# Performance work log

Measured on AMD Instinct MI355X. Metric: run time of the kernel, lower is better.

The kernel has to match this reference:

```python
import jax, jax.numpy as jnp
import numpy as np
from math import factorial as fact

H = 32            # hidden channels
NUM_GRAPHS = 128  # number of graphs in the batch (fill_max of `batch`)
SIGMA = 0.1       # gaussian basis width
MUS = jnp.asarray(np.linspace(0.7, 1.7, 10), jnp.float32)
R_CUT = 1.5       # polynomial cutoff radius (p=6)
SL = {0: (0, 1), 1: (1, 4), 2: (4, 9)}  # m-slices per degree in flattened (l,m) layout

# ---- real Clebsch-Gordan coefficients (computed once in numpy) ----

def _cg1(l1, m1, l2, m2, l3, m3):
    if m1 + m2 != m3:
        return 0.0
    pref = ((2 * l3 + 1) * fact(l3 + l1 - l2) * fact(l3 - l1 + l2) * fact(l1 + l2 - l3) / fact(l1 + l2 + l3 + 1)) ** 0.5
    pref *= (fact(l3 + m3) * fact(l3 - m3) * fact(l1 - m1) * fact(l1 + m1) * fact(l2 - m2) * fact(l2 + m2)) ** 0.5
    s = 0.0
    for k in range(0, l1 + l2 - l3 + 1):
        d = [k, l1 + l2 - l3 - k, l1 - m1 - k, l2 + m2 - k, l3 - l2 + m1 + k, l3 - l1 - m2 + k]
        if min(d) < 0:
            continue
        s += (-1.0) ** k / np.prod([float(fact(v)) for v in d])
    return pref * s

def _q(l):  # complex -> real spherical-harmonic basis change
    Q = np.zeros((2 * l + 1, 2 * l + 1), dtype=complex)
    Q[l, l] = 1.0
    for m in range(1, l + 1):
        Q[l + m, l + m] = (-1) ** m / np.sqrt(2)
        Q[l + m, l - m] = 1 / np.sqrt(2)
        Q[l - m, l - m] = 1j / np.sqrt(2)
        Q[l - m, l + m] = -1j * (-1) ** m / np.sqrt(2)
    return Q

def _real_cg(l1, l2, l3):
    Cc = np.zeros((2 * l1 + 1, 2 * l2 + 1, 2 * l3 + 1))
    for m1 in range(-l1, l1 + 1):
        for m2 in range(-l2, l2 + 1):
            m3 = m1 + m2
            if abs(m3) <= l3:
                Cc[m1 + l1, m2 + l2, m3 + l3] = _cg1(l1, m1, l2, m2, l3, m3)
    C = np.einsum('ai,bj,ck,ijk->abc', _q(l1), _q(l2), np.conj(_q(l3)), Cc)
    if np.abs(C.imag).max() > np.abs(C.real).max():
        C = C * (-1j)
    return jnp.asarray(np.real(C), dtype=jnp.float32)

PATHS1 = [(0, 0, 0), (0, 1, 1)]
PATHS2 = [(0, 0, 0), (0, 1, 1), (1, 0, 1), (1, 1, 0), (1, 1, 1), (1, 2, 1)]
PATHS3 = [(0, 0, 0), (1, 1, 0)]
CG = {p: _real_cg(*p) for p in set(PATHS1 + PATHS2 + PATHS3)}

# ---- module math ----

def _ssp(x):  # shifted softplus
    return jax.nn.softplus(x) - jnp.asarray(np.log(2.0), x.dtype)

def _norm_act(h):  # NormAct(ShiftedSoftPlus, L=1): act scalars, gate l=1 vectors by act(norm)/norm
    s = _ssp(h[:, :1, :])
    v = h[:, 1:4, :]
    n = jnp.sqrt(jnp.sum(v * v, axis=1, keepdims=True) + 1e-12)
    return jnp.concatenate([s, v * (_ssp(n) / n)], axis=1)

def _tfn(x, src, dst, edge_sh, w, ew, paths, L_out, channel_wise, N):
    # x: (N, M_in, C_in); per edge: gather x_j, CG tensor product with edge SH,
    # radial weights, cutoff weighting, scatter-sum to destination nodes.
    E = edge_sh.shape[0]
    C_out = w.shape[-1]
    M_out = (L_out + 1) ** 2
    xj = x[src]  # (E, M_in, C_in) edge gather
    msg = jnp.zeros((E, M_out, C_out), x.dtype)
    for p, (l1, l2, l3) in enumerate(paths):
        x1 = xj[:, SL[l1][0]:SL[l1][1], :]          # (E, 2l1+1, C_in)
        y2 = edge_sh[:, SL[l2][0]:SL[l2][1]]        # (E, 2l2+1)
        t = jnp.einsum('abc,eai,eb->eci', CG[(l1, l2, l3)], x1, y2)  # (E, 2l3+1, C_in)
        if channel_wise:
            t = t * w[:, p, None, :]                # (E, P, C) radial weights
        else:
            t = jnp.einsum('eci,eio->eco', t, w[:, p])  # (E, P, C_in, C_out)
        msg = msg.at[:, SL[l3][0]:SL[l3][1], :].add(t * ew[:, None, None])
    return jax.ops.segment_sum(msg, dst, num_segments=N)

def _forward(x, edge_index, edge_sh, edge_len, batch, W1, b1, W2, b2, W3, b3, Wo, bo):
    N = x.shape[0]
    src, dst = edge_index[0], edge_index[1]
    d = edge_len
    emb = jnp.exp(-((d[:, None] - MUS) ** 2) / (2.0 * SIGMA ** 2))  # (E, 10)
    u = d / R_CUT
    ew = jnp.where(u < 1.0, 1.0 - 28.0 * u ** 6 + 48.0 * u ** 7 - 21.0 * u ** 8, 0.0)
    w1 = (emb @ W1 + b1).reshape(-1, 2, 1, H)   # channel_wise=False: (E,P,Cin,Cout)
    w2 = (emb @ W2 + b2).reshape(-1, 6, H)      # channel_wise=True
    w3 = (emb @ W3 + b3).reshape(-1, 2, H)
    h = x[:, None, :]  # (N, 1, 1): L_in=0 scalars
    h = _norm_act(_tfn(h, src, dst, edge_sh, w1, ew, PATHS1, 1, False, N))
    h = _norm_act(_tfn(h, src, dst, edge_sh, w2, ew, PATHS2, 1, True, N))
    h = jax.nn.silu(_tfn(h, src, dst, edge_sh, w3, ew, PATHS3, 0, True, N))
    g = jax.ops.segment_sum(h[:, 0, :], batch, num_segments=NUM_GRAPHS)  # (B, H)
    return jax.nn.softmax(g @ Wo + bo, axis=-1)

def setup_inputs() -> dict:
    N, E = 50000, 800000
    ks = jax.random.split(jax.random.key(0), 16)
    inp = {
        'x': jax.random.normal(ks[0], (N, 1), jnp.float32),
        'edge_index': jax.random.randint(ks[1], (2, E), 0, N),
        'edge_sh': jax.random.normal(ks[2], (E, 9), jnp.float32),
        'edge_len': jax.random.uniform(ks[3], (E,), jnp.float32),
        'batch': jnp.sort(jax.random.randint(ks[4], (N,), 0, NUM_GRAPHS)),
        'W1': jax.random.normal(ks[5], (10, 2 * H), jnp.float32) * 0.1,
        'b1': jnp.zeros((2 * H,), jnp.float32),
        'W2': jax.random.normal(ks[6], (10, 6 * H), jnp.float32) * 0.1,
        'b2': jnp.zeros((6 * H,), jnp.float32),
        'W3': jax.random.normal(ks[7], (10, 2 * H), jnp.float32) * 0.1,
        'b3': jnp.zeros((2 * H,), jnp.float32),
        'Wo': jax.random.normal(ks[8], (H, 8), jnp.float32) * 0.1,
        'bo': jnp.zeros((8,), jnp.float32),
    }
    return inp

def reference(x, edge_sh, edge_len, W1, b1, W2, b2, W3, b3, Wo, bo, edge_index, batch):
    return _forward(x, edge_index, edge_sh, edge_len, batch, W1, b1, W2, b2, W3, b3, Wo, bo)
```

## Files before the change

### kernel.cpp

```cpp
#include <hip/hip_runtime.h>
#include <cmath>
#include <cstring>
#include <complex>

#define HCH 32

struct CGT {
  float c000;
  float c011[9];
  float c101[9];
  float c110[9];
  float c111[27];
  float c121[45];
};

static double factd(int n){ double r=1.0; for(int i=2;i<=n;++i) r*=i; return r; }

static double cg1(int l1,int m1,int l2,int m2,int l3,int m3){
  if(m1+m2!=m3) return 0.0;
  double pref = std::sqrt((2*l3+1)*factd(l3+l1-l2)*factd(l3-l1+l2)*factd(l1+l2-l3)/factd(l1+l2+l3+1));
  pref *= std::sqrt(factd(l3+m3)*factd(l3-m3)*factd(l1-m1)*factd(l1+m1)*factd(l2-m2)*factd(l2+m2));
  double s=0.0;
  for(int k=0;k<=l1+l2-l3;++k){
    int d[6]={k, l1+l2-l3-k, l1-m1-k, l2+m2-k, l3-l2+m1+k, l3-l1-m2+k};
    bool neg=false; for(int i=0;i<6;i++) if(d[i]<0) neg=true;
    if(neg) continue;
    double prod=1.0; for(int i=0;i<6;i++) prod*=factd(d[i]);
    s += ((k&1)? -1.0:1.0)/prod;
  }
  return pref*s;
}

static void qmat(int l, std::complex<double> Q[5][5]){
  for(int i=0;i<5;i++) for(int j=0;j<5;j++) Q[i][j]=0.0;
  Q[l][l]=1.0;
  const double is2 = 1.0/std::sqrt(2.0);
  for(int m=1;m<=l;m++){
    double sgn = (m&1)? -1.0: 1.0;
    Q[l+m][l+m] = sgn*is2;
    Q[l+m][l-m] = is2;
    Q[l-m][l-m] = std::complex<double>(0.0, is2);
    Q[l-m][l+m] = std::complex<double>(0.0, -sgn*is2);
  }
}

static void real_cg(int l1,int l2,int l3, float* out){
  int n1=2*l1+1, n2=2*l2+1, n3=2*l3+1;
  double Cc[5][5][5];
  std::memset(Cc,0,sizeof Cc);
  for(int m1=-l1;m1<=l1;m1++) for(int m2=-l2;m2<=l2;m2++){
    int m3=m1+m2;
    if(m3>=-l3 && m3<=l3) Cc[m1+l1][m2+l2][m3+l3]=cg1(l1,m1,l2,m2,l3,m3);
  }
  std::complex<double> Q1[5][5],Q2[5][5],Q3[5][5];
  qmat(l1,Q1); qmat(l2,Q2); qmat(l3,Q3);
  std::complex<double> C[5][5][5];
  double maxre=0.0, maxim=0.0;
  for(int a=0;a<n1;a++) for(int b=0;b<n2;b++) for(int c=0;c<n3;c++){
    std::complex<double> s=0.0;
    for(int i=0;i<n1;i++) for(int j=0;j<n2;j++) for(int k=0;k<n3;k++){
      double cc=Cc[i][j][k];
      if(cc!=0.0) s += Q1[a][i]*Q2[b][j]*std::conj(Q3[c][k])*cc;
    }
    C[a][b][c]=s;
    maxre=std::max(maxre,std::fabs(s.real()));
    maxim=std::max(maxim,std::fabs(s.imag()));
  }
  bool flip = maxim>maxre;
  for(int a=0;a<n1;a++) for(int b=0;b<n2;b++) for(int c=0;c<n3;c++){
    std::complex<double> v=C[a][b][c];
    if(flip) v *= std::complex<double>(0.0,-1.0);
    out[(a*n2+b)*n3+c]=(float)v.real();
  }
}

static void build_cg(CGT* cg){
  float t000[1];  real_cg(0,0,0,t000); cg->c000=t000[0];
  real_cg(0,1,1,cg->c011);
  real_cg(1,0,1,cg->c101);
  real_cg(1,1,0,cg->c110);
  real_cg(1,1,1,cg->c111);
  real_cg(1,2,1,cg->c121);
}

__device__ __forceinline__ float sspf(float x){
  return fmaxf(x,0.0f) + __logf(1.0f + __expf(-fabsf(x))) - 0.69314718055994530942f;
}

__device__ __forceinline__ float edge_env_inline(float d, float* emb){
#pragma unroll
  for(int k=0;k<10;k++){
    float t = d - (0.7f + (float)k*(1.0f/9.0f));
    emb[k] = __expf(-t*t*50.0f);
  }
  float u = d*(1.0f/1.5f);
  if(u >= 1.0f) return 0.0f;
  float u2=u*u, u3=u2*u, u6=u3*u3, u7=u6*u, u8=u7*u;
  return 1.0f - 28.0f*u6 + 48.0f*u7 - 21.0f*u8;
}

__global__ void deg_kernel(const int* __restrict__ ei, int* __restrict__ deg, int E){
  int e = blockIdx.x*blockDim.x + threadIdx.x;
  if(e >= E) return;
  atomicAdd(&deg[ei[E+e]], 1);
}

__global__ void scanA_kernel(const int* __restrict__ deg, int* __restrict__ rowptr,
                             int* __restrict__ bsum, int N){
  __shared__ int sm[256];
  int t = threadIdx.x, b = blockIdx.x, i = b*256 + t;
  int v = (i < N) ? deg[i] : 0;
  sm[t] = v;
  __syncthreads();
  for(int off=1; off<256; off<<=1){
    int add = (t >= off) ? sm[t-off] : 0;
    __syncthreads();
    sm[t] += add;
    __syncthreads();
  }
  if(i < N) rowptr[i] = sm[t] - v;
  if(t == 255) bsum[b] = sm[255];
}

__global__ void scanB_kernel(int* __restrict__ bsum, int* __restrict__ rowptr, int nb, int N){
  __shared__ int sm[256];
  int t = threadIdx.x;
  int v = (t < nb) ? bsum[t] : 0;
  sm[t] = v;
  __syncthreads();
  for(int off=1; off<256; off<<=1){
    int add = (t >= off) ? sm[t-off] : 0;
    __syncthreads();
    sm[t] += add;
    __syncthreads();
  }
  if(t < nb) bsum[t] = sm[t] - v;
  if(t == 255) rowptr[N] = sm[255];
}

__global__ void scanC_kernel(int* __restrict__ rowptr, const int* __restrict__ bsum, int N){
  int i = blockIdx.x*blockDim.x + threadIdx.x;
  if(i < N) rowptr[i] += bsum[i>>8];
}

__global__ void fill_kernel(const int* __restrict__ ei, const float* __restrict__ elen,
                            const float* __restrict__ sh,
                            const int* __restrict__ rowptr, int* __restrict__ fillc,
                            float* __restrict__ pedge, int E){
  int e = blockIdx.x*blockDim.x + threadIdx.x;
  if(e >= E) return;
  int dst = ei[E+e];
  int p = atomicAdd(&fillc[dst], 1);
  size_t slot = (size_t)rowptr[dst] + p;
  const float* she = sh + (size_t)e*9;
  float4* pd = (float4*)pedge + slot*3;
  pd[0] = make_float4(elen[e], __int_as_float(ei[e]), she[0], she[1]);
  pd[1] = make_float4(she[2], she[3], she[4], she[5]);
  pd[2] = make_float4(she[6], she[7], she[8], 0.f);
}


__global__ __launch_bounds__(256, 4)
void g1_kernel(const float* __restrict__ x,
               const float* __restrict__ pedge,
               const int* __restrict__ rowptr,
               const float* __restrict__ W1, const float* __restrict__ b1,
               float* __restrict__ out, int N, CGT cg){
  int t = blockIdx.x*blockDim.x + threadIdx.x;
  int n = t >> 5, h = t & 31;
  if(n >= N) return;
  int beg = rowptr[n], end = rowptr[n+1];
  float Wr0[10], Wr1[10];
#pragma unroll
  for(int k=0;k<10;k++){ Wr0[k] = W1[k*64 + h]; Wr1[k] = W1[k*64 + HCH + h]; }
  float bb0 = b1[h], bb1 = b1[HCH+h];
  float a0=0.f, a1=0.f, a2=0.f, a3=0.f;
  const float4* pe = (const float4*)pedge;
  for(int i=beg;i<end;i++){
    float4 r0 = pe[(size_t)i*3+0];
    float4 r1 = pe[(size_t)i*3+1];
    float em[10];
    float ew = edge_env_inline(r0.x, em);
    int src = __float_as_int(r0.y);
    float w0 = bb0, w1v = bb1;
#pragma unroll
    for(int k=0;k<10;k++){ w0 += em[k]*Wr0[k]; w1v += em[k]*Wr1[k]; }
    float base = x[src]*ew;
    a0 += cg.c000*base*r0.z*w0;
    float bw = base*w1v;
    a1 += (cg.c011[0]*r0.w + cg.c011[3]*r1.x + cg.c011[6]*r1.y)*bw;
    a2 += (cg.c011[1]*r0.w + cg.c011[4]*r1.x + cg.c011[7]*r1.y)*bw;
    a3 += (cg.c011[2]*r0.w + cg.c011[5]*r1.x + cg.c011[8]*r1.y)*bw;
  }
  float ss = a1*a1 + a2*a2 + a3*a3 + 1e-12f;
  float rn = rsqrtf(ss);
  float sc = sspf(ss*rn)*rn;
  float* p = out + (size_t)n*128;
  p[h]       = sspf(a0);
  p[HCH+h]   = a1*sc;
  p[2*HCH+h] = a2*sc;
  p[3*HCH+h] = a3*sc;
}

__global__ __launch_bounds__(256, 4)
void g2_kernel(const float* __restrict__ hin,
               const float* __restrict__ pedge,
               const int* __restrict__ rowptr,
               const float* __restrict__ W2, const float* __restrict__ b2,
               float* __restrict__ out, int N, CGT cg){
  int t = blockIdx.x*blockDim.x + threadIdx.x;
  int n = t >> 5, h = t & 31;
  if(n >= N) return;
  int beg = rowptr[n], end = rowptr[n+1];
  float Wr[60];
#pragma unroll
  for(int k=0;k<10;k++)
#pragma unroll
    for(int p=0;p<6;p++) Wr[k*6+p] = W2[k*192 + p*HCH + h];
  float bb[6];
#pragma unroll
  for(int p=0;p<6;p++) bb[p] = b2[p*HCH + h];
  float a0=0.f, a1=0.f, a2=0.f, a3=0.f;
  const float4* pe = (const float4*)pedge;
  for(int i=beg;i<end;i++){
    float4 r0 = pe[(size_t)i*3+0];
    float4 r1 = pe[(size_t)i*3+1];
    float4 r2 = pe[(size_t)i*3+2];
    float em[10];
    float ew = edge_env_inline(r0.x, em);
    int src = __float_as_int(r0.y);
    float w_[6];
#pragma unroll
    for(int p=0;p<6;p++) w_[p] = bb[p];
#pragma unroll
    for(int k=0;k<10;k++)
#pragma unroll
      for(int p=0;p<6;p++) w_[p] += em[k]*Wr[k*6+p];
    const float* hn = hin + (size_t)src*128;
    float x0  = hn[h];
    float xv0 = hn[HCH+h], xv1 = hn[2*HCH+h], xv2 = hn[3*HCH+h];
    float s0  = r0.z;
    float sv0 = r0.w, sv1 = r1.x, sv2 = r1.y;
    float s2v[5] = { r1.z, r1.w, r2.x, r2.y, r2.z };

    float m0 = 0.0f, m1 = 0.0f, m2 = 0.0f, m3 = 0.0f;
    m0 += cg.c000 * x0 * s0 * w_[0];
    {
      float xw = x0 * w_[1];
      m1 += (cg.c011[0]*sv0 + cg.c011[3]*sv1 + cg.c011[6]*sv2)*xw;
      m2 += (cg.c011[1]*sv0 + cg.c011[4]*sv1 + cg.c011[7]*sv2)*xw;
      m3 += (cg.c011[2]*sv0 + cg.c011[5]*sv1 + cg.c011[8]*sv2)*xw;
    }
    {
      float sw = s0 * w_[2];
      m1 += (cg.c101[0]*xv0 + cg.c101[3]*xv1 + cg.c101[6]*xv2)*sw;
      m2 += (cg.c101[1]*xv0 + cg.c101[4]*xv1 + cg.c101[7]*xv2)*sw;
      m3 += (cg.c101[2]*xv0 + cg.c101[5]*xv1 + cg.c101[8]*xv2)*sw;
    }
    {
      float tt = cg.c110[0]*xv0*sv0 + cg.c110[1]*xv0*sv1 + cg.c110[2]*xv0*sv2
               + cg.c110[3]*xv1*sv0 + cg.c110[4]*xv1*sv1 + cg.c110[5]*xv1*sv2
               + cg.c110[6]*xv2*sv0 + cg.c110[7]*xv2*sv1 + cg.c110[8]*xv2*sv2;
      m0 += tt * w_[3];
    }
    {
      float xvv[3] = {xv0, xv1, xv2};
      float svv[3] = {sv0, sv1, sv2};
      float t1=0.f, t2=0.f, t3=0.f;
#pragma unroll
      for(int a=0;a<3;a++)
#pragma unroll
        for(int b=0;b<3;b++){
          float xs = xvv[a]*svv[b];
          t1 += cg.c111[(a*3+b)*3+0]*xs;
          t2 += cg.c111[(a*3+b)*3+1]*xs;
          t3 += cg.c111[(a*3+b)*3+2]*xs;
        }
      m1 += t1*w_[4]; m2 += t2*w_[4]; m3 += t3*w_[4];
    }
    {
      float xvv[3] = {xv0, xv1, xv2};
      float t1=0.f, t2=0.f, t3=0.f;
#pragma unroll
      for(int a=0;a<3;a++)
#pragma unroll
        for(int b=0;b<5;b++){
          float xs = xvv[a]*s2v[b];
          t1 += cg.c121[(a*5+b)*3+0]*xs;
          t2 += cg.c121[(a*5+b)*3+1]*xs;
          t3 += cg.c121[(a*5+b)*3+2]*xs;
        }
      m1 += t1*w_[5]; m2 += t2*w_[5]; m3 += t3*w_[5];
    }
    a0 += m0*ew; a1 += m1*ew; a2 += m2*ew; a3 += m3*ew;
  }
  float ss = a1*a1 + a2*a2 + a3*a3 + 1e-12f;
  float rn = rsqrtf(ss);
  float sc = sspf(ss*rn)*rn;
  float* p = out + (size_t)n*128;
  p[h]       = sspf(a0);
  p[HCH+h]   = a1*sc;
  p[2*HCH+h] = a2*sc;
  p[3*HCH+h] = a3*sc;
}

__global__ __launch_bounds__(256, 4)
void g3_kernel(const float* __restrict__ hin,
               const float* __restrict__ pedge,
               const int* __restrict__ rowptr,
               const int* __restrict__ batch,
               const float* __restrict__ W3, const float* __restrict__ b3,
               float* __restrict__ g, int N, CGT cg){
  int t = blockIdx.x*blockDim.x + threadIdx.x;
  int n = t >> 5, h = t & 31;
  if(n >= N) return;
  int beg = rowptr[n], end = rowptr[n+1];
  float Wr0[10], Wr1[10];
#pragma unroll
  for(int k=0;k<10;k++){ Wr0[k] = W3[k*64 + h]; Wr1[k] = W3[k*64 + HCH + h]; }
  float bb0 = b3[h], bb1 = b3[HCH+h];
  float acc = 0.f;
  const float4* pe = (const float4*)pedge;
  for(int i=beg;i<end;i++){
    float4 r0 = pe[(size_t)i*3+0];
    float4 r1 = pe[(size_t)i*3+1];
    float em[10];
    float ew = edge_env_inline(r0.x, em);
    int src = __float_as_int(r0.y);
    float w0 = bb0, w1v = bb1;
#pragma unroll
    for(int k=0;k<10;k++){ w0 += em[k]*Wr0[k]; w1v += em[k]*Wr1[k]; }
    const float* hn = hin + (size_t)src*128;
    float x0 = hn[h];
    float xv0 = hn[HCH+h], xv1 = hn[2*HCH+h], xv2 = hn[3*HCH+h];
    float m = cg.c000 * x0 * r0.z * w0;
    float tt = cg.c110[0]*xv0*r0.w + cg.c110[1]*xv0*r1.x + cg.c110[2]*xv0*r1.y
             + cg.c110[3]*xv1*r0.w + cg.c110[4]*xv1*r1.x + cg.c110[5]*xv1*r1.y
             + cg.c110[6]*xv2*r0.w + cg.c110[7]*xv2*r1.x + cg.c110[8]*xv2*r1.y;
    m += tt * w1v;
    acc += m*ew;
  }
  float si = acc*__frcp_rn(1.0f + __expf(-acc));
  atomicAdd(&g[(size_t)batch[n]*HCH + h], si);
}

__global__ void l1_kernel(const float* __restrict__ x, const int* __restrict__ ei,
                          const float* __restrict__ sh, const float* __restrict__ elen,
                          const float* __restrict__ W1, const float* __restrict__ b1,
                          float* __restrict__ acc, int E, CGT cg){
  int t = blockIdx.x*blockDim.x + threadIdx.x;
  int e = t >> 5, h = t & 31;
  if(e >= E) return;
  float emb[10];
  float ew = edge_env_inline(elen[e], emb);
  int src = ei[e], dst = ei[E+e];
  float w0 = b1[h], w1v = b1[HCH+h];
#pragma unroll
  for(int k=0;k<10;k++){
    w0  += emb[k]*W1[k*64 + h];
    w1v += emb[k]*W1[k*64 + HCH + h];
  }
  const float* she = sh + (size_t)e*9;
  float base = x[src]*ew;
  float* ad = acc + (size_t)dst*128;
  atomicAdd(&ad[h], cg.c000*base*she[0]*w0);
  float bw = base*w1v;
  atomicAdd(&ad[HCH+h],   (cg.c011[0]*she[1] + cg.c011[3]*she[2] + cg.c011[6]*she[3])*bw);
  atomicAdd(&ad[2*HCH+h], (cg.c011[1]*she[1] + cg.c011[4]*she[2] + cg.c011[7]*she[3])*bw);
  atomicAdd(&ad[3*HCH+h], (cg.c011[2]*she[1] + cg.c011[5]*she[2] + cg.c011[8]*she[3])*bw);
}

__global__ void normact_kernel(float* __restrict__ buf, int N){
  int t = blockIdx.x*blockDim.x + threadIdx.x;
  int n = t >> 5, h = t & 31;
  if(n >= N) return;
  float* p = buf + (size_t)n*128;
  float s  = p[h];
  float v1 = p[HCH+h], v2 = p[2*HCH+h], v3 = p[3*HCH+h];
  float ss = v1*v1 + v2*v2 + v3*v3 + 1e-12f;
  float rn = rsqrtf(ss);
  float sc = sspf(ss*rn)*rn;
  p[h]       = sspf(s);
  p[HCH+h]   = v1*sc;
  p[2*HCH+h] = v2*sc;
  p[3*HCH+h] = v3*sc;
}

__global__ void l2_kernel(const float* __restrict__ hin, const int* __restrict__ ei,
                          const float* __restrict__ sh, const float* __restrict__ elen,
                          const float* __restrict__ W2, const float* __restrict__ b2,
                          float* __restrict__ acc, int E, CGT cg){
  int t = blockIdx.x*blockDim.x + threadIdx.x;
  int e = t >> 5, h = t & 31;
  if(e >= E) return;
  float emb[10];
  float ew = edge_env_inline(elen[e], emb);
  int src = ei[e], dst = ei[E+e];
  float w[6];
#pragma unroll
  for(int p=0;p<6;p++) w[p] = b2[p*HCH + h];
#pragma unroll
  for(int k=0;k<10;k++){
    float ek = emb[k];
    const float* Wr = W2 + k*192;
#pragma unroll
    for(int p=0;p<6;p++) w[p] += ek*Wr[p*HCH + h];
  }
  const float* hn = hin + (size_t)src*128;
  float x0 = hn[h];
  float xv[3] = { hn[HCH+h], hn[2*HCH+h], hn[3*HCH+h] };
  const float* she = sh + (size_t)e*9;
  float s0 = she[0];
  float sv[3]  = { she[1], she[2], she[3] };
  float s2v[5] = { she[4], she[5], she[6], she[7], she[8] };
  float m0 = 0.0f, m[3] = {0.0f,0.0f,0.0f};
  m0 += cg.c000 * x0 * s0 * w[0];
#pragma unroll
  for(int c=0;c<3;c++){
    float tc = cg.c011[0*3+c]*sv[0] + cg.c011[1*3+c]*sv[1] + cg.c011[2*3+c]*sv[2];
    m[c] += tc * x0 * w[1];
  }
#pragma unroll
  for(int c=0;c<3;c++){
    float tc = cg.c101[0*3+c]*xv[0] + cg.c101[1*3+c]*xv[1] + cg.c101[2*3+c]*xv[2];
    m[c] += tc * s0 * w[2];
  }
  {
    float tt=0.0f;
#pragma unroll
    for(int a=0;a<3;a++)
#pragma unroll
      for(int b=0;b<3;b++) tt += cg.c110[a*3+b]*xv[a]*sv[b];
    m0 += tt * w[3];
  }
#pragma unroll
  for(int c=0;c<3;c++){
    float tt=0.0f;
#pragma unroll
    for(int a=0;a<3;a++)
#pragma unroll
      for(int b=0;b<3;b++) tt += cg.c111[(a*3+b)*3+c]*xv[a]*sv[b];
    m[c] += tt * w[4];
  }
#pragma unroll
  for(int c=0;c<3;c++){
    float tt=0.0f;
#pragma unroll
    for(int a=0;a<3;a++)
#pragma unroll
      for(int b=0;b<5;b++) tt += cg.c121[(a*5+b)*3+c]*xv[a]*s2v[b];
    m[c] += tt * w[5];
  }
  float* ad = acc + (size_t)dst*128;
  atomicAdd(&ad[h], m0*ew);
#pragma unroll
  for(int c=0;c<3;c++) atomicAdd(&ad[(1+c)*HCH + h], m[c]*ew);
}

__global__ void l3_kernel(const float* __restrict__ hin, const int* __restrict__ ei,
                          const float* __restrict__ sh, const float* __restrict__ elen,
                          const float* __restrict__ W3, const float* __restrict__ b3,
                          float* __restrict__ acc, int E, CGT cg){
  int t = blockIdx.x*blockDim.x + threadIdx.x;
  int e = t >> 5, h = t & 31;
  if(e >= E) return;
  float emb[10];
  float ew = edge_env_inline(elen[e], emb);
  int src = ei[e], dst = ei[E+e];
  float w0 = b3[h], w1v = b3[HCH+h];
#pragma unroll
  for(int k=0;k<10;k++){
    w0  += emb[k]*W3[k*64 + h];
    w1v += emb[k]*W3[k*64 + HCH + h];
  }
  const float* hn = hin + (size_t)src*128;
  float x0 = hn[h];
  float xv[3] = { hn[HCH+h], hn[2*HCH+h], hn[3*HCH+h] };
  const float* she = sh + (size_t)e*9;
  float m = cg.c000 * x0 * she[0] * w0;
  float tt = cg.c110[0]*xv[0]*she[1] + cg.c110[1]*xv[0]*she[2] + cg.c110[2]*xv[0]*she[3]
           + cg.c110[3]*xv[1]*she[1] + cg.c110[4]*xv[1]*she[2] + cg.c110[5]*xv[1]*she[3]
           + cg.c110[6]*xv[2]*she[1] + cg.c110[7]*xv[2]*she[2] + cg.c110[8]*xv[2]*she[3];
  m += tt * w1v;
  atomicAdd(&acc[(size_t)dst*HCH + h], m*ew);
}

__global__ void pool_kernel(const float* __restrict__ acc, const int* __restrict__ batch,
                            float* __restrict__ g, int N){
  int t = blockIdx.x*blockDim.x + threadIdx.x;
  int n = t >> 5, h = t & 31;
  if(n >= N) return;
  float v = acc[(size_t)n*HCH + h];
  float si = v*__frcp_rn(1.0f + __expf(-v));
  atomicAdd(&g[(size_t)batch[n]*HCH + h], si);
}

__global__ void head_kernel(const float* __restrict__ g, const float* __restrict__ Wo,
                            const float* __restrict__ bo, float* __restrict__ out){
  int gi = threadIdx.x;
  if(gi >= 128) return;
  float logit[8];
#pragma unroll
  for(int o=0;o<8;o++) logit[o] = bo[o];
  for(int hh=0; hh<HCH; hh++){
    float gv = g[gi*HCH + hh];
#pragma unroll
    for(int o=0;o<8;o++) logit[o] += gv*Wo[hh*8 + o];
  }
  float mx = logit[0];
#pragma unroll
  for(int o=1;o<8;o++) mx = fmaxf(mx, logit[o]);
  float ex[8]; float s=0.0f;
#pragma unroll
  for(int o=0;o<8;o++){ ex[o]=__expf(logit[o]-mx); s+=ex[o]; }
  float inv = 1.0f/s;
#pragma unroll
  for(int o=0;o<8;o++) out[gi*8 + o] = ex[o]*inv;
}

extern "C" void kernel_launch(void* const* d_in, const int* in_sizes, int n_in,
                              void* d_out, int out_size, void* d_ws, size_t ws_size,
                              hipStream_t stream){
  const float* x    = (const float*)d_in[0];
  const int*   ei   = (const int*)  d_in[1];
  const float* sh   = (const float*)d_in[2];
  const float* elen = (const float*)d_in[3];
  const int*   batch= (const int*)  d_in[4];
  const float* W1   = (const float*)d_in[5];
  const float* b1   = (const float*)d_in[6];
  const float* W2   = (const float*)d_in[7];
  const float* b2   = (const float*)d_in[8];
  const float* W3   = (const float*)d_in[9];
  const float* b3   = (const float*)d_in[10];
  const float* Wo   = (const float*)d_in[11];
  const float* bo   = (const float*)d_in[12];
  int N = in_sizes[0];
  int E = in_sizes[3];

  CGT cg; build_cg(&cg);

  int nb = (N + 255)/256;

  float* pedge  = (float*)d_ws;
  float* bufA   = pedge + (size_t)E*12;
  float* bufB   = bufA + (size_t)N*128;
  float* g      = bufB + (size_t)N*128;
  int*   deg    = (int*)(g + 128*HCH);
  int*   fillc  = deg + N;
  int*   rowptr = fillc + N;
  int*   bsum   = rowptr + (N+1);

  size_t csr_b = ((size_t)E*12 + (size_t)N*128*2 + 128*HCH)*sizeof(float)
               + ((size_t)3*N + 1 + 256)*sizeof(int);
  bool use_csr = (ws_size >= csr_b) && (nb <= 256);

  dim3 blk(256);
  int eblk1   = (E + 255)/256;
  int eblocks = (int)(((long long)E*HCH + 255)/256);
  int nblocks = (int)(((long long)N*HCH + 255)/256);

  if(use_csr){
    hipMemsetAsync(g, 0, (size_t)(128*HCH)*sizeof(float) + (size_t)2*N*sizeof(int), stream);
    deg_kernel <<<eblk1, blk, 0, stream>>>(ei, deg, E);
    scanA_kernel<<<nb, blk, 0, stream>>>(deg, rowptr, bsum, N);
    scanB_kernel<<<1, blk, 0, stream>>>(bsum, rowptr, nb, N);
    scanC_kernel<<<nb, blk, 0, stream>>>(rowptr, bsum, N);
    fill_kernel<<<eblk1, blk, 0, stream>>>(ei, elen, sh, rowptr, fillc, pedge, E);
    g1_kernel<<<nblocks, blk, 0, stream>>>(x, pedge, rowptr, W1, b1, bufA, N, cg);
    g2_kernel<<<nblocks, blk, 0, stream>>>(bufA, pedge, rowptr, W2, b2, bufB, N, cg);
    g3_kernel<<<nblocks, blk, 0, stream>>>(bufB, pedge, rowptr, batch, W3, b3, g, N, cg);
    head_kernel<<<1, 128, 0, stream>>>(g, Wo, bo, (float*)d_out);
  } else {
    float* fbufA = (float*)d_ws;
    float* fbufB = fbufA + (size_t)N*128;
    float* fbufC = fbufB + (size_t)N*128;
    float* fg    = fbufC + (size_t)N*HCH;
    size_t base_b = ((size_t)N*128*2 + (size_t)N*HCH + 128*HCH)*sizeof(float);
    hipMemsetAsync(d_ws, 0, base_b, stream);
    l1_kernel<<<eblocks, blk, 0, stream>>>(x, ei, sh, elen, W1, b1, fbufA, E, cg);
    normact_kernel<<<nblocks, blk, 0, stream>>>(fbufA, N);
    l2_kernel<<<eblocks, blk, 0, stream>>>(fbufA, ei, sh, elen, W2, b2, fbufB, E, cg);
    normact_kernel<<<nblocks, blk, 0, stream>>>(fbufB, N);
    l3_kernel<<<eblocks, blk, 0, stream>>>(fbufB, ei, sh, elen, W3, b3, fbufC, E, cg);
    pool_kernel<<<nblocks, blk, 0, stream>>>(fbufC, batch, fg, N);
    head_kernel<<<1, 128, 0, stream>>>(fg, Wo, bo, (float*)d_out);
  }
}
```

Before: 727.6 us.

## Split each node's edge list across two half-waves with prefetch and shuffle reduce

The g1/g2/g3 gather kernels now assign one 64-lane wavefront per node instead of 32 lanes. Each half-wave processes alternate edges, prefetches the next edge record into registers while computing the current one, and combines partial sums with a cross-half shuffle before one half writes the output. This doubles thread-level parallelism over edges and shortens per-node serial chains. The cost is twice as many threads and blocks, duplicated weight-register loads, and idle lanes on low-degree nodes.

```diff
diff --git a/kernel.cpp b/kernel.cpp
--- a/kernel.cpp
+++ b/kernel.cpp
@@ -166,9 +166,11 @@
                const int* __restrict__ rowptr,
                const float* __restrict__ W1, const float* __restrict__ b1,
                float* __restrict__ out, int N, CGT cg){
-  int t = blockIdx.x*blockDim.x + threadIdx.x;
-  int n = t >> 5, h = t & 31;
+  int tid = blockIdx.x*blockDim.x + threadIdx.x;
+  int n = tid >> 6;
   if(n >= N) return;
+  int lane = threadIdx.x & 63;
+  int h = lane & 31, j = lane >> 5;
   int beg = rowptr[n], end = rowptr[n+1];
   float Wr0[10], Wr1[10];
 #pragma unroll
@@ -176,9 +178,13 @@
   float bb0 = b1[h], bb1 = b1[HCH+h];
   float a0=0.f, a1=0.f, a2=0.f, a3=0.f;
   const float4* pe = (const float4*)pedge;
-  for(int i=beg;i<end;i++){
-    float4 r0 = pe[(size_t)i*3+0];
-    float4 r1 = pe[(size_t)i*3+1];
+  int i = beg + j;
+  float4 r0, r1;
+  if(i < end){ r0 = pe[(size_t)i*3+0]; r1 = pe[(size_t)i*3+1]; }
+  while(i < end){
+    int inx = i + 2;
+    float4 n0, n1;
+    if(inx < end){ n0 = pe[(size_t)inx*3+0]; n1 = pe[(size_t)inx*3+1]; }
     float em[10];
     float ew = edge_env_inline(r0.x, em);
     int src = __float_as_int(r0.y);
@@ -191,15 +197,22 @@
     a1 += (cg.c011[0]*r0.w + cg.c011[3]*r1.x + cg.c011[6]*r1.y)*bw;
     a2 += (cg.c011[1]*r0.w + cg.c011[4]*r1.x + cg.c011[7]*r1.y)*bw;
     a3 += (cg.c011[2]*r0.w + cg.c011[5]*r1.x + cg.c011[8]*r1.y)*bw;
-  }
-  float ss = a1*a1 + a2*a2 + a3*a3 + 1e-12f;
-  float rn = rsqrtf(ss);
-  float sc = sspf(ss*rn)*rn;
-  float* p = out + (size_t)n*128;
-  p[h]       = sspf(a0);
-  p[HCH+h]   = a1*sc;
-  p[2*HCH+h] = a2*sc;
-  p[3*HCH+h] = a3*sc;
+    r0 = n0; r1 = n1; i = inx;
+  }
+  a0 += __shfl_xor(a0, 32);
+  a1 += __shfl_xor(a1, 32);
+  a2 += __shfl_xor(a2, 32);
+  a3 += __shfl_xor(a3, 32);
+  if(j == 0){
+    float ss = a1*a1 + a2*a2 + a3*a3 + 1e-12f;
+    float rn = rsqrtf(ss);
+    float sc = sspf(ss*rn)*rn;
+    float* p = out + (size_t)n*128;
+    p[h]       = sspf(a0);
+    p[HCH+h]   = a1*sc;
+    p[2*HCH+h] = a2*sc;
+    p[3*HCH+h] = a3*sc;
+  }
 }
 
 __global__ __launch_bounds__(256, 4)
@@ -208,9 +221,11 @@
                const int* __restrict__ rowptr,
                const float* __restrict__ W2, const float* __restrict__ b2,
                float* __restrict__ out, int N, CGT cg){
-  int t = blockIdx.x*blockDim.x + threadIdx.x;
-  int n = t >> 5, h = t & 31;
+  int tid = blockIdx.x*blockDim.x + threadIdx.x;
+  int n = tid >> 6;
   if(n >= N) return;
+  int lane = threadIdx.x & 63;
+  int h = lane & 31, j = lane >> 5;
   int beg = rowptr[n], end = rowptr[n+1];
   float Wr[60];
 #pragma unroll
@@ -222,10 +237,13 @@
   for(int p=0;p<6;p++) bb[p] = b2[p*HCH + h];
   float a0=0.f, a1=0.f, a2=0.f, a3=0.f;
   const float4* pe = (const float4*)pedge;
-  for(int i=beg;i<end;i++){
-    float4 r0 = pe[(size_t)i*3+0];
-    float4 r1 = pe[(size_t)i*3+1];
-    float4 r2 = pe[(size_t)i*3+2];
+  int i = beg + j;
+  float4 r0, r1, r2;
+  if(i < end){ r0 = pe[(size_t)i*3+0]; r1 = pe[(size_t)i*3+1]; r2 = pe[(size_t)i*3+2]; }
+  while(i < end){
+    int inx = i + 2;
+    float4 n0, n1, n2;
+    if(inx < end){ n0 = pe[(size_t)inx*3+0]; n1 = pe[(size_t)inx*3+1]; n2 = pe[(size_t)inx*3+2]; }
     float em[10];
     float ew = edge_env_inline(r0.x, em);
     int src = __float_as_int(r0.y);
@@ -293,15 +311,22 @@
       m1 += t1*w_[5]; m2 += t2*w_[5]; m3 += t3*w_[5];
     }
     a0 += m0*ew; a1 += m1*ew; a2 += m2*ew; a3 += m3*ew;
-  }
-  float ss = a1*a1 + a2*a2 + a3*a3 + 1e-12f;
-  float rn = rsqrtf(ss);
-  float sc = sspf(ss*rn)*rn;
-  float* p = out + (size_t)n*128;
-  p[h]       = sspf(a0);
-  p[HCH+h]   = a1*sc;
-  p[2*HCH+h] = a2*sc;
-  p[3*HCH+h] = a3*sc;
+    r0 = n0; r1 = n1; r2 = n2; i = inx;
+  }
+  a0 += __shfl_xor(a0, 32);
+  a1 += __shfl_xor(a1, 32);
+  a2 += __shfl_xor(a2, 32);
+  a3 += __shfl_xor(a3, 32);
+  if(j == 0){
+    float ss = a1*a1 + a2*a2 + a3*a3 + 1e-12f;
+    float rn = rsqrtf(ss);
+    float sc = sspf(ss*rn)*rn;
+    float* p = out + (size_t)n*128;
+    p[h]       = sspf(a0);
+    p[HCH+h]   = a1*sc;
+    p[2*HCH+h] = a2*sc;
+    p[3*HCH+h] = a3*sc;
+  }
 }
 
 __global__ __launch_bounds__(256, 4)
@@ -311,9 +336,11 @@
                const int* __restrict__ batch,
                const float* __restrict__ W3, const float* __restrict__ b3,
                float* __restrict__ g, int N, CGT cg){
-  int t = blockIdx.x*blockDim.x + threadIdx.x;
-  int n = t >> 5, h = t & 31;
+  int tid = blockIdx.x*blockDim.x + threadIdx.x;
+  int n = tid >> 6;
   if(n >= N) return;
+  int lane = threadIdx.x & 63;
+  int h = lane & 31, j = lane >> 5;
   int beg = rowptr[n], end = rowptr[n+1];
   float Wr0[10], Wr1[10];
 #pragma unroll
@@ -321,9 +348,13 @@
   float bb0 = b3[h], bb1 = b3[HCH+h];
   float acc = 0.f;
   const float4* pe = (const float4*)pedge;
-  for(int i=beg;i<end;i++){
-    float4 r0 = pe[(size_t)i*3+0];
-    float4 r1 = pe[(size_t)i*3+1];
+  int i = beg + j;
+  float4 r0, r1;
+  if(i < end){ r0 = pe[(size_t)i*3+0]; r1 = pe[(size_t)i*3+1]; }
+  while(i < end){
+    int inx = i + 2;
+    float4 n0, n1;
+    if(inx < end){ n0 = pe[(size_t)inx*3+0]; n1 = pe[(size_t)inx*3+1]; }
     float em[10];
     float ew = edge_env_inline(r0.x, em);
     int src = __float_as_int(r0.y);
@@ -339,9 +370,13 @@
              + cg.c110[6]*xv2*r0.w + cg.c110[7]*xv2*r1.x + cg.c110[8]*xv2*r1.y;
     m += tt * w1v;
     acc += m*ew;
-  }
-  float si = acc*__frcp_rn(1.0f + __expf(-acc));
-  atomicAdd(&g[(size_t)batch[n]*HCH + h], si);
+    r0 = n0; r1 = n1; i = inx;
+  }
+  acc += __shfl_xor(acc, 32);
+  if(j == 0){
+    float si = acc*__frcp_rn(1.0f + __expf(-acc));
+    atomicAdd(&g[(size_t)batch[n]*HCH + h], si);
+  }
 }
 
 __global__ void l1_kernel(const float* __restrict__ x, const int* __restrict__ ei,
@@ -558,6 +593,7 @@
   int eblk1   = (E + 255)/256;
   int eblocks = (int)(((long long)E*HCH + 255)/256);
   int nblocks = (int)(((long long)N*HCH + 255)/256);
+  int wblocks = (int)(((long long)N*64 + 255)/256);
 
   if(use_csr){
     hipMemsetAsync(g, 0, (size_t)(128*HCH)*sizeof(float) + (size_t)2*N*sizeof(int), stream);
@@ -566,9 +602,9 @@
     scanB_kernel<<<1, blk, 0, stream>>>(bsum, rowptr, nb, N);
     scanC_kernel<<<nb, blk, 0, stream>>>(rowptr, bsum, N);
     fill_kernel<<<eblk1, blk, 0, stream>>>(ei, elen, sh, rowptr, fillc, pedge, E);
-    g1_kernel<<<nblocks, blk, 0, stream>>>(x, pedge, rowptr, W1, b1, bufA, N, cg);
-    g2_kernel<<<nblocks, blk, 0, stream>>>(bufA, pedge, rowptr, W2, b2, bufB, N, cg);
-    g3_kernel<<<nblocks, blk, 0, stream>>>(bufB, pedge, rowptr, batch, W3, b3, g, N, cg);
+    g1_kernel<<<wblocks, blk, 0, stream>>>(x, pedge, rowptr, W1, b1, bufA, N, cg);
+    g2_kernel<<<wblocks, blk, 0, stream>>>(bufA, pedge, rowptr, W2, b2, bufB, N, cg);
+    g3_kernel<<<wblocks, blk, 0, stream>>>(bufB, pedge, rowptr, batch, W3, b3, g, N, cg);
     head_kernel<<<1, 128, 0, stream>>>(g, Wo, bo, (float*)d_out);
   } else {
     float* fbufA = (float*)d_ws;
```

Result: slower. 746.0 us (+2.5%).
